# Optimization experiments

Hardware: AMD Instinct MI355X
Metric: run time of the kernel (lower is better)

The kernel has to match this reference:

```python
import jax, jax.numpy as jnp
import numpy as np

V, E, H, B, S = 50000, 300, 256, 64, 512  # vocab, embed, hidden, batch, max seq len


def setup_inputs() -> dict:
    key = jax.random.key(0)
    ks = jax.random.split(key, 5)
    return dict(
        input_inds=jax.random.randint(ks[0], (B, S), 0, V),
        input_lens=jax.random.randint(ks[1], (B,), 1, S + 1),
        emb_table=jax.random.normal(ks[2], (V, E), jnp.float32) * 0.1,
        w_ih=jax.random.normal(ks[3], (3 * H, E), jnp.float32) * (1.0 / np.sqrt(E)),
        w_hh=jax.random.normal(ks[4], (3 * H, H), jnp.float32) * (1.0 / np.sqrt(H)),
        b_ih=jnp.zeros((3 * H,), jnp.float32),
        b_hh=jnp.zeros((3 * H,), jnp.float32),
    )


def _gru(x, lens, w_ih, w_hh, b_ih, b_hh):
    """Batched masked GRU (PyTorch gate order r, z, n). x: [B,S,E]."""
    Hh = w_hh.shape[1]
    # precompute input-to-hidden gates for all steps: [B,S,3H]
    gx = jnp.einsum('bse,ge->bsg', x, w_ih) + b_ih

    def step(h, inputs):
        gx_t, t = inputs                       # gx_t: [B,3H]
        gh = h @ w_hh.T + b_hh                 # [B,3H]
        r = jax.nn.sigmoid(gx_t[:, :Hh] + gh[:, :Hh])
        z = jax.nn.sigmoid(gx_t[:, Hh:2 * Hh] + gh[:, Hh:2 * Hh])
        n = jnp.tanh(gx_t[:, 2 * Hh:] + r * gh[:, 2 * Hh:])
        h_new = (1.0 - z) * n + z * h
        valid = (t < lens)[:, None]            # freeze state past each sample's length
        h = jnp.where(valid, h_new, h)
        return h, h

    h0 = jnp.zeros((x.shape[0], Hh), x.dtype)
    hT, hs = jax.lax.scan(step, h0, (gx.transpose(1, 0, 2), jnp.arange(x.shape[1])))
    return hs.transpose(1, 0, 2), hT           # [B,S,H], [B,H]


def reference(input_inds, input_lens, emb_table, w_ih, w_hh, b_ih, b_hh):
    mask = (jnp.arange(S)[None, :] < input_lens[:, None]).astype(jnp.float32)  # [B,S]
    emb = emb_table[input_inds] * mask[..., None]                              # zero-padded embeddings
    feats, hT = _gru(emb, input_lens, w_ih, w_hh, b_ih, b_hh)
    feats = feats * mask[..., None]                                            # zero-pad outputs past len
    hiddens = hT[None]                                                         # (num_layers*dirs=1, B, H)
    return emb, feats, mask, hiddens
```

## Files before the change

kernel.cpp:

```cpp
#include <hip/hip_runtime.h>

#define B_ 64
#define S_ 512
#define E_ 300
#define H_ 256
#define G_ 768

typedef _Float16 h2_t __attribute__((ext_vector_type(2)));

__device__ __forceinline__ unsigned pack_h2(float a, float b) {
  h2_t v;
  v.x = (_Float16)a;
  v.y = (_Float16)b;
  return __builtin_bit_cast(unsigned, v);
}

__device__ __forceinline__ float fdot2f(unsigned w, unsigned h, float acc) {
#if __has_builtin(__builtin_amdgcn_fdot2)
  return __builtin_amdgcn_fdot2(__builtin_bit_cast(h2_t, w),
                                __builtin_bit_cast(h2_t, h), acc, false);
#else
  h2_t wv = __builtin_bit_cast(h2_t, w), hv = __builtin_bit_cast(h2_t, h);
  return acc + (float)wv.x * (float)hv.x + (float)wv.y * (float)hv.y;
#endif
}

__global__ void k_embed(const int* __restrict__ inds, const int* __restrict__ lens,
                        const float* __restrict__ table, float* __restrict__ out_emb,
                        float* __restrict__ out_mask) {
  const long total = (long)B_ * S_ * E_;
  for (long idx = (long)blockIdx.x * blockDim.x + threadIdx.x; idx < total;
       idx += (long)gridDim.x * blockDim.x) {
    int row = (int)(idx / E_);
    int e = (int)(idx - (long)row * E_);
    int b = row >> 9;
    int s = row & 511;
    bool valid = s < lens[b];
    float v = 0.0f;
    if (valid) v = table[(long)inds[row] * E_ + e];
    out_emb[idx] = v;
    if (e == 0) out_mask[row] = valid ? 1.0f : 0.0f;
  }
}

#define KC 30
__global__ __launch_bounds__(256) void k_gx(const float* __restrict__ A,
                                            const float* __restrict__ W,
                                            const float* __restrict__ bias,
                                            _Float16* __restrict__ gx) {
  __shared__ float As[KC][132];
  __shared__ float Ws[KC][132];
  const int tid = threadIdx.x;
  const int row0 = blockIdx.x * 128;
  const int col0 = blockIdx.y * 128;
  const int tx = tid & 15;
  const int ty = tid >> 4;

  float acc[8][8];
#pragma unroll
  for (int i = 0; i < 8; ++i)
#pragma unroll
    for (int j = 0; j < 8; ++j) acc[i][j] = 0.0f;

  for (int kt = 0; kt < E_ / KC; ++kt) {
    const int k0 = kt * KC;
#pragma unroll
    for (int u = 0; u < 15; ++u) {
      int idx = tid + u * 256;
      int r = idx / KC;
      int kk = idx - r * KC;
      As[kk][r] = A[(long)(row0 + r) * E_ + k0 + kk];
      Ws[kk][r] = W[(long)(col0 + r) * E_ + k0 + kk];
    }
    __syncthreads();
    for (int kk = 0; kk < KC; ++kk) {
      float4 a0 = *(const float4*)&As[kk][ty * 4];
      float4 a1 = *(const float4*)&As[kk][64 + ty * 4];
      float4 b0 = *(const float4*)&Ws[kk][tx * 4];
      float4 b1 = *(const float4*)&Ws[kk][64 + tx * 4];
      float av[8] = {a0.x, a0.y, a0.z, a0.w, a1.x, a1.y, a1.z, a1.w};
      float bv[8] = {b0.x, b0.y, b0.z, b0.w, b1.x, b1.y, b1.z, b1.w};
#pragma unroll
      for (int i = 0; i < 8; ++i)
#pragma unroll
        for (int j = 0; j < 8; ++j) acc[i][j] += av[i] * bv[j];
    }
    __syncthreads();
  }

#pragma unroll
  for (int i = 0; i < 8; ++i) {
    int r = row0 + ((i < 4) ? (ty * 4 + i) : (64 + ty * 4 + i - 4));
#pragma unroll
    for (int j = 0; j < 8; ++j) {
      int c = col0 + ((j < 4) ? (tx * 4 + j) : (64 + tx * 4 + j - 4));
      gx[(long)r * G_ + c] = (_Float16)(acc[i][j] + bias[c]);
    }
  }
}

__global__ __launch_bounds__(512, 2) void k_gru(
    const float* __restrict__ w_hh, const float* __restrict__ b_hh,
    const int* __restrict__ lens, const _Float16* __restrict__ gx,
    float* __restrict__ feats, float* __restrict__ hid) {
  const int b = blockIdx.x;
  const int j = threadIdx.x;
  const int len = lens[b];

  __shared__ unsigned h2buf[128];
  __shared__ float ghbuf[G_];

  const int p = j >> 1;
  const int hf = j & 1;
  const int hf64 = hf * 64;

  unsigned wreg[192];
#pragma unroll
  for (int r = 0; r < 3; ++r) {
    const float* src = w_hh + (long)(3 * p + r) * H_ + 128 * hf;
#pragma unroll
    for (int c2 = 0; c2 < 32; ++c2) {
      float4 f = *(const float4*)(src + 4 * c2);
      wreg[r * 64 + 2 * c2] = pack_h2(f.x, f.y);
      wreg[r * 64 + 2 * c2 + 1] = pack_h2(f.z, f.w);
    }
  }

  float bias_r = 0.f, bias_z = 0.f, bias_n = 0.f, hreg = 0.0f;
  if (j < H_) {
    bias_r = b_hh[j];
    bias_z = b_hh[j + H_];
    bias_n = b_hh[j + 2 * H_];
  }

  if (j < 128) h2buf[j] = 0u;
  __syncthreads();

  const _Float16* gxb = gx + (long)b * S_ * G_;

  for (int t = 0; t < len; ++t) {
    float a0 = 0.f, a1 = 0.f, a2 = 0.f;
#pragma unroll
    for (int c = 0; c < 16; ++c) {
      float4 hv = *(const float4*)&h2buf[hf64 + c * 4];
      unsigned h0 = __builtin_bit_cast(unsigned, hv.x);
      unsigned h1 = __builtin_bit_cast(unsigned, hv.y);
      unsigned h2v = __builtin_bit_cast(unsigned, hv.z);
      unsigned h3 = __builtin_bit_cast(unsigned, hv.w);
      a0 = fdot2f(wreg[c * 4 + 0], h0, a0);
      a0 = fdot2f(wreg[c * 4 + 1], h1, a0);
      a0 = fdot2f(wreg[c * 4 + 2], h2v, a0);
      a0 = fdot2f(wreg[c * 4 + 3], h3, a0);
      a1 = fdot2f(wreg[64 + c * 4 + 0], h0, a1);
      a1 = fdot2f(wreg[64 + c * 4 + 1], h1, a1);
      a1 = fdot2f(wreg[64 + c * 4 + 2], h2v, a1);
      a1 = fdot2f(wreg[64 + c * 4 + 3], h3, a1);
      a2 = fdot2f(wreg[128 + c * 4 + 0], h0, a2);
      a2 = fdot2f(wreg[128 + c * 4 + 1], h1, a2);
      a2 = fdot2f(wreg[128 + c * 4 + 2], h2v, a2);
      a2 = fdot2f(wreg[128 + c * 4 + 3], h3, a2);
    }
    a0 += __shfl_xor(a0, 1);
    a1 += __shfl_xor(a1, 1);
    a2 += __shfl_xor(a2, 1);
    if (hf == 0) {
      ghbuf[3 * p] = a0;
      ghbuf[3 * p + 2] = a2;
    } else {
      ghbuf[3 * p + 1] = a1;
    }
    __syncthreads();

    if (j < H_) {
      const _Float16* gxt = gxb + (long)t * G_;
      float gxr = (float)gxt[j];
      float gxz = (float)gxt[j + H_];
      float gxn = (float)gxt[j + 2 * H_];
      float ghr = ghbuf[j] + bias_r;
      float ghz = ghbuf[j + H_] + bias_z;
      float ghn = ghbuf[j + 2 * H_] + bias_n;
      float r = 1.0f / (1.0f + __expf(-(gxr + ghr)));
      float z = 1.0f / (1.0f + __expf(-(gxz + ghz)));
      float n = tanhf(gxn + r * ghn);
      hreg = (1.0f - z) * n + z * hreg;
      feats[((long)b * S_ + t) * H_ + j] = hreg;
      float other = __shfl_xor(hreg, 1);
      if (!(j & 1)) h2buf[j >> 1] = pack_h2(hreg, other);
    }
    __syncthreads();
  }

  {
    const long tail = (long)(S_ - len) * H_;
    float* dst = feats + ((long)b * S_ + len) * H_;
    for (long idx = j; idx < tail; idx += 512) dst[idx] = 0.0f;
  }
  if (j < H_) hid[b * H_ + j] = hreg;
}

extern "C" void kernel_launch(void* const* d_in, const int* in_sizes, int n_in,
                              void* d_out, int out_size, void* d_ws, size_t ws_size,
                              hipStream_t stream) {
  const int* inds = (const int*)d_in[0];
  const int* lens = (const int*)d_in[1];
  const float* table = (const float*)d_in[2];
  const float* w_ih = (const float*)d_in[3];
  const float* w_hh = (const float*)d_in[4];
  const float* b_ih = (const float*)d_in[5];
  const float* b_hh = (const float*)d_in[6];

  float* out = (float*)d_out;
  float* out_emb = out;
  float* out_feats = out + (long)B_ * S_ * E_;
  float* out_mask = out_feats + (long)B_ * S_ * H_;
  float* out_hid = out_mask + (long)B_ * S_;

  _Float16* gx = (_Float16*)d_ws;

  k_embed<<<2048, 256, 0, stream>>>(inds, lens, table, out_emb, out_mask);
  dim3 g2(32768 / 128, G_ / 128);
  k_gx<<<g2, 256, 0, stream>>>(out_emb, w_ih, b_ih, gx);
  k_gru<<<B_, 512, 0, stream>>>(w_hh, b_hh, lens, gx, out_feats, out_hid);
}
```

Measured before the change: 915.1 us.

## Fuse GRU gate math into matvec threads with double-buffered hidden state

Each thread pair now owns one hidden unit for all three gates (r,z,n rows regrouped by gate), so the gate nonlinearity is computed right after the shuffle reduction. This removes the ghbuf shared-memory round trip and one of the two __syncthreads per timestep, using a double-buffered h2buf instead. The gx values for the next step are prefetched during the current step's matvec. Launch bounds drop to one block per CU, which gives the compiler more register room. Both threads of a pair now compute the gate math redundantly.

```diff
diff --git a/kernel.cpp b/kernel.cpp
--- a/kernel.cpp
+++ b/kernel.cpp
@@ -99,7 +99,7 @@
   }
 }
 
-__global__ __launch_bounds__(512, 2) void k_gru(
+__global__ __launch_bounds__(512, 1) void k_gru(
     const float* __restrict__ w_hh, const float* __restrict__ b_hh,
     const int* __restrict__ lens, const _Float16* __restrict__ gx,
     float* __restrict__ feats, float* __restrict__ hid) {
@@ -107,8 +107,7 @@
   const int j = threadIdx.x;
   const int len = lens[b];
 
-  __shared__ unsigned h2buf[128];
-  __shared__ float ghbuf[G_];
+  __shared__ unsigned h2buf[2][128];
 
   const int p = j >> 1;
   const int hf = j & 1;
@@ -116,33 +115,41 @@
 
   unsigned wreg[192];
 #pragma unroll
-  for (int r = 0; r < 3; ++r) {
-    const float* src = w_hh + (long)(3 * p + r) * H_ + 128 * hf;
+  for (int g = 0; g < 3; ++g) {
+    const float* src = w_hh + ((long)g * H_ + p) * H_ + 128 * hf;
 #pragma unroll
     for (int c2 = 0; c2 < 32; ++c2) {
       float4 f = *(const float4*)(src + 4 * c2);
-      wreg[r * 64 + 2 * c2] = pack_h2(f.x, f.y);
-      wreg[r * 64 + 2 * c2 + 1] = pack_h2(f.z, f.w);
-    }
-  }
-
-  float bias_r = 0.f, bias_z = 0.f, bias_n = 0.f, hreg = 0.0f;
-  if (j < H_) {
-    bias_r = b_hh[j];
-    bias_z = b_hh[j + H_];
-    bias_n = b_hh[j + 2 * H_];
-  }
-
-  if (j < 128) h2buf[j] = 0u;
+      wreg[g * 64 + 2 * c2] = pack_h2(f.x, f.y);
+      wreg[g * 64 + 2 * c2 + 1] = pack_h2(f.z, f.w);
+    }
+  }
+
+  const float bias_r = b_hh[p];
+  const float bias_z = b_hh[H_ + p];
+  const float bias_n = b_hh[2 * H_ + p];
+  float hreg = 0.0f;
+
+  if (j < 128) h2buf[0][j] = 0u;
   __syncthreads();
 
   const _Float16* gxb = gx + (long)b * S_ * G_;
-
+  float gxr = (float)gxb[p];
+  float gxz = (float)gxb[H_ + p];
+  float gxn = (float)gxb[2 * H_ + p];
+
+  int cur = 0;
   for (int t = 0; t < len; ++t) {
+    const int tn = (t + 1 < len) ? (t + 1) : t;
+    const _Float16* gxt = gxb + (long)tn * G_;
+    _Float16 nr = gxt[p];
+    _Float16 nz = gxt[H_ + p];
+    _Float16 nn = gxt[2 * H_ + p];
+
     float a0 = 0.f, a1 = 0.f, a2 = 0.f;
 #pragma unroll
     for (int c = 0; c < 16; ++c) {
-      float4 hv = *(const float4*)&h2buf[hf64 + c * 4];
+      float4 hv = *(const float4*)&h2buf[cur][hf64 + c * 4];
       unsigned h0 = __builtin_bit_cast(unsigned, hv.x);
       unsigned h1 = __builtin_bit_cast(unsigned, hv.y);
       unsigned h2v = __builtin_bit_cast(unsigned, hv.z);
@@ -163,31 +170,22 @@
     a0 += __shfl_xor(a0, 1);
     a1 += __shfl_xor(a1, 1);
     a2 += __shfl_xor(a2, 1);
-    if (hf == 0) {
-      ghbuf[3 * p] = a0;
-      ghbuf[3 * p + 2] = a2;
-    } else {
-      ghbuf[3 * p + 1] = a1;
-    }
+
+    float r = 1.0f / (1.0f + __expf(-(gxr + a0 + bias_r)));
+    float z = 1.0f / (1.0f + __expf(-(gxz + a1 + bias_z)));
+    float n = tanhf(gxn + r * (a2 + bias_n));
+    hreg = (1.0f - z) * n + z * hreg;
+
+    if (hf == 0) feats[((long)b * S_ + t) * H_ + p] = hreg;
+
+    float hother = __shfl_xor(hreg, 2);
+    if ((j & 3) == 0) h2buf[cur ^ 1][j >> 2] = pack_h2(hreg, hother);
+
     __syncthreads();
-
-    if (j < H_) {
-      const _Float16* gxt = gxb + (long)t * G_;
-      float gxr = (float)gxt[j];
-      float gxz = (float)gxt[j + H_];
-      float gxn = (float)gxt[j + 2 * H_];
-      float ghr = ghbuf[j] + bias_r;
-      float ghz = ghbuf[j + H_] + bias_z;
-      float ghn = ghbuf[j + 2 * H_] + bias_n;
-      float r = 1.0f / (1.0f + __expf(-(gxr + ghr)));
-      float z = 1.0f / (1.0f + __expf(-(gxz + ghz)));
-      float n = tanhf(gxn + r * ghn);
-      hreg = (1.0f - z) * n + z * hreg;
-      feats[((long)b * S_ + t) * H_ + j] = hreg;
-      float other = __shfl_xor(hreg, 1);
-      if (!(j & 1)) h2buf[j >> 1] = pack_h2(hreg, other);
-    }
-    __syncthreads();
+    cur ^= 1;
+    gxr = (float)nr;
+    gxz = (float)nz;
+    gxn = (float)nn;
   }
 
   {
@@ -195,7 +193,7 @@
     float* dst = feats + ((long)b * S_ + len) * H_;
     for (long idx = j; idx < tail; idx += 512) dst[idx] = 0.0f;
   }
-  if (j < H_) hid[b * H_ + j] = hreg;
+  if (hf == 0) hid[b * H_ + p] = hreg;
 }
 
 extern "C" void kernel_launch(void* const* d_in, const int* in_sizes, int n_in,
```

Result: faster. 835.3 us (-8.7%).
